# Optimization experiments

Measured on AMD Instinct MI355X. Metric: run time of the kernel, lower is better.

Reference implementation:

```python
import jax, jax.numpy as jnp
import numpy as np

NUM_HEADS = 16
DK = 64
DV = 64
MASK_FILL = -10000000000.0


def setup_inputs() -> dict:
    key = jax.random.key(0)
    kq, kk, kv, km = jax.random.split(key, 4)
    B, L, D = 2, 2048, NUM_HEADS * DK
    Q = jax.random.normal(kq, (B, L, D), dtype=jnp.float32)
    K = jax.random.normal(kk, (B, L, D), dtype=jnp.float32)
    V = jax.random.normal(kv, (B, L, NUM_HEADS * DV), dtype=jnp.float32)
    mask = jax.random.randint(km, (B, L, L), 0, 2).astype(jnp.bool_)
    return {"Q": Q, "K": K, "V": V, "mask": mask}


def reference(Q, K, V, mask):
    B, Lq, _ = Q.shape
    Lk = K.shape[1]
    # split heads: [B, H, L, d]
    q = Q.reshape(B, Lq, NUM_HEADS, DK).transpose(0, 2, 1, 3)
    k = K.reshape(B, Lk, NUM_HEADS, DK).transpose(0, 2, 1, 3)
    v = V.reshape(B, Lk, NUM_HEADS, DV).transpose(0, 2, 1, 3)
    # scores [B, H, Lq, Lk]; NOTE: original masks BEFORE scaling by 1/sqrt(dk)
    scores = jnp.einsum("bhqd,bhkd->bhqk", q, k)
    scores = jnp.where(mask[:, None, :, :], MASK_FILL, scores)
    scores = scores / jnp.sqrt(jnp.asarray(DK, dtype=scores.dtype))
    attn = jax.nn.softmax(scores, axis=-1)
    out = jnp.einsum("bhqk,bhkd->bhqd", attn, v)  # [B, H, Lq, dv]
    # concat heads back: [B, Lq, H*dv]
    return out.transpose(0, 2, 1, 3).reshape(B, Lq, NUM_HEADS * DV)
```

## Files before the change

### kernel.cpp

```cpp
#include <hip/hip_runtime.h>
#include <hip/hip_bf16.h>

#define NH 16
#define DH 64
#define LL 2048
#define DM 1024
#define SCALE2 0.1803368801111204f
#define GUARD_HI 60.0f
#define NT64 16

typedef __attribute__((ext_vector_type(4))) float f32x4;
typedef __attribute__((ext_vector_type(16))) float f32x16;
typedef __attribute__((ext_vector_type(8))) short bf16x8;

__device__ __forceinline__ unsigned pk2(float lo, float hi) {
    __hip_bfloat162 h = __float22bfloat162_rn(make_float2(lo, hi));
    union { __hip_bfloat162 h; unsigned u; } c; c.h = h; return c.u;
}
__device__ __forceinline__ bf16x8 cvt8(float4 a, float4 b) {
    union { bf16x8 v; unsigned u[4]; } r;
    r.u[0] = pk2(a.x, a.y); r.u[1] = pk2(a.z, a.w);
    r.u[2] = pk2(b.x, b.y); r.u[3] = pk2(b.z, b.w);
    return r.v;
}
__device__ __forceinline__ float exp2_fast(float x) {
    float y;
    asm("v_exp_f32 %0, %1" : "=v"(y) : "v"(x));
    return y;
}
__device__ __forceinline__ float keepf(float p, unsigned nw, int idx) {
    int k = (int)(nw << (31 - idx)) >> 31;
    unsigned pu = __builtin_bit_cast(unsigned, p) & (unsigned)k;
    return __builtin_bit_cast(float, pu);
}

__global__ __launch_bounds__(256) void pack_mask(const void* __restrict__ mask,
                                                 unsigned* __restrict__ bits)
{
    const int tid = threadIdx.x;
    const int lane = tid & 63;
    const int* mw = (const int*)mask;
    unsigned long long bad = __ballot((unsigned)mw[lane] > 1u);
    const bool is_int = (bad == 0ULL);

    const int wid = blockIdx.x * 256 + tid;
    const int kw = wid & 63;
    const int q64 = wid >> 6;
    unsigned m = 0;
    if (is_int) {
        const int* p = (const int*)mask + (size_t)q64 * LL + kw * 32;
        #pragma unroll
        for (int j = 0; j < 32; j += 4) {
            int4 v = *(const int4*)(p + j);
            m |= (v.x ? 1u : 0u) << j;
            m |= (v.y ? 1u : 0u) << (j + 1);
            m |= (v.z ? 1u : 0u) << (j + 2);
            m |= (v.w ? 1u : 0u) << (j + 3);
        }
    } else {
        const unsigned* p = (const unsigned*)((const unsigned char*)mask
                                              + (size_t)q64 * LL + kw * 32);
        #pragma unroll
        for (int j = 0; j < 8; ++j) {
            unsigned v = p[j];
            m |= (v & 1u) << (4 * j);
            m |= ((v >> 8) & 1u) << (4 * j + 1);
            m |= ((v >> 16) & 1u) << (4 * j + 2);
            m |= ((v >> 24) & 1u) << (4 * j + 3);
        }
    }
    bits[wid] = ~m;
}

__global__ __launch_bounds__(256) void prep_k(const float* __restrict__ K,
                                              short* __restrict__ Kb)
{
    const int kt = blockIdx.x, h = blockIdx.y, b = blockIdx.z;
    const int tid = threadIdx.x;
    const int key = tid >> 2;
    const int d16 = tid & 3;
    const float* src = K + ((size_t)b * LL + kt * 64 + key) * DM + h * DH + d16 * 16;
    float4 f0 = *(const float4*)(src);
    float4 f1 = *(const float4*)(src + 4);
    float4 f2 = *(const float4*)(src + 8);
    float4 f3 = *(const float4*)(src + 12);
    short* dst = Kb + (((size_t)(b * NH + h) * 32 + kt) << 12);
    const int base = d16 * 1024 + (key >> 5) * 512 + (key & 31) * 8;
    *(bf16x8*)&dst[base] = cvt8(f0, f1);
    *(bf16x8*)&dst[base + 256] = cvt8(f2, f3);
}

__global__ __launch_bounds__(256) void prep_v(const float* __restrict__ V,
                                              short* __restrict__ Vb)
{
    const int kt = blockIdx.x, h = blockIdx.y, b = blockIdx.z;
    const int tid = threadIdx.x;
    const int kp = tid & 31;
    const int dv8 = tid >> 5;
    const float* s0 = V + ((size_t)b * LL + kt * 64 + 2 * kp) * DM + h * DH + dv8 * 8;
    float4 a0 = *(const float4*)(s0);
    float4 a1 = *(const float4*)(s0 + 4);
    float4 b0 = *(const float4*)(s0 + DM);
    float4 b1 = *(const float4*)(s0 + DM + 4);
    float av[8] = {a0.x, a0.y, a0.z, a0.w, a1.x, a1.y, a1.z, a1.w};
    float bv[8] = {b0.x, b0.y, b0.z, b0.w, b1.x, b1.y, b1.z, b1.w};
    short* dst = Vb + (((size_t)(b * NH + h) * 32 + kt) << 12);
    const int key0 = 2 * kp;
    const int m = key0 >> 4;
    const int w16 = key0 & 15;
    const int hh = (w16 >> 2) & 1;
    const int i0 = (w16 & 3) + 4 * (w16 >> 3);
    #pragma unroll
    for (int j = 0; j < 8; ++j) {
        int dv = dv8 * 8 + j;
        int off = m * 1024 + (dv >> 5) * 512 + hh * 256 + (dv & 31) * 8 + i0;
        *(unsigned*)&dst[off] = pk2(av[j], bv[j]);
    }
}

__global__ __launch_bounds__(512, 4) void mha_fwd6(
    const float* __restrict__ Q, const short* __restrict__ Kb,
    const short* __restrict__ Vb, const unsigned* __restrict__ mbits,
    float* __restrict__ out)
{
    const int bid = blockIdx.x;
    const int xcd = bid & 7;
    const int j = bid >> 3;
    const int pair = xcd * 4 + (j >> 4);
    const int qblk = j & 15;
    const int hd = pair & 15;
    const int b = pair >> 4;

    const int tid = threadIdx.x;
    const int w = tid >> 6;
    const int g = w >> 2;
    const int wg = w & 3;
    const int lane = tid & 63;
    const int lq = lane & 31;
    const int hh = lane >> 5;

    const int qbase = qblk * 128 + wg * 32;

    __shared__ short smem[32768];
    #define KOFF(gg, cc) (((gg) * 2 + (cc)) * 4096)
    #define VOFF(gg, cc) (16384 + ((gg) * 2 + (cc)) * 4096)

    const short* Ktile0 = Kb + ((size_t)(b * NH + hd) << 17);
    const short* Vtile0 = Vb + ((size_t)(b * NH + hd) << 17);
    const unsigned* Mrow = mbits + ((size_t)b * LL + qbase + lq) * 64 + g * 32;

    uint2 mreg = *(const uint2*)(Mrow);
    {
        const short* kb_ = Ktile0 + (size_t)(g * 16) * 4096;
        const short* vb_ = Vtile0 + (size_t)(g * 16) * 4096;
        #pragma unroll
        for (int c = 0; c < 2; ++c) {
            __builtin_amdgcn_global_load_lds(
                (const unsigned*)(kb_ + wg * 1024 + c * 512 + lane * 8),
                (unsigned*)&smem[KOFF(g, 0) + wg * 1024 + c * 512], 16, 0, 0);
            __builtin_amdgcn_global_load_lds(
                (const unsigned*)(vb_ + wg * 1024 + c * 512 + lane * 8),
                (unsigned*)&smem[VOFF(g, 0) + wg * 1024 + c * 512], 16, 0, 0);
        }
    }

    bf16x8 qf[4];
    {
        const float* qp = Q + ((size_t)b * LL + qbase + lq) * DM + hd * DH + 8 * hh;
        #pragma unroll
        for (int d16 = 0; d16 < 4; ++d16) {
            float4 a = *(const float4*)(qp + 16 * d16);
            float4 c = *(const float4*)(qp + 16 * d16 + 4);
            a.x *= SCALE2; a.y *= SCALE2; a.z *= SCALE2; a.w *= SCALE2;
            c.x *= SCALE2; c.y *= SCALE2; c.z *= SCALE2; c.w *= SCALE2;
            qf[d16] = cvt8(a, c);
        }
    }

    f32x16 o0, o1;
    #pragma unroll
    for (int i = 0; i < 16; ++i) { o0[i] = 0.f; o1[i] = 0.f; }
    float l_own = 0.f;
    float m_shift = 0.f;
    const int sh4 = 4 * hh;

    asm volatile("s_waitcnt vmcnt(0)" ::: "memory");
    __builtin_amdgcn_s_barrier();

    #pragma unroll 2
    for (int t = 0; t < NT64; ++t) {
        const int cur = t & 1;
        const uint2 m2 = mreg;
        if (t + 1 < NT64) {
            mreg = *(const uint2*)(Mrow + 2 * (t + 1));
            const short* kb_ = Ktile0 + (size_t)(g * 16 + t + 1) * 4096;
            const short* vb_ = Vtile0 + (size_t)(g * 16 + t + 1) * 4096;
            #pragma unroll
            for (int c = 0; c < 2; ++c) {
                __builtin_amdgcn_global_load_lds(
                    (const unsigned*)(kb_ + wg * 1024 + c * 512 + lane * 8),
                    (unsigned*)&smem[KOFF(g, cur ^ 1) + wg * 1024 + c * 512], 16, 0, 0);
                __builtin_amdgcn_global_load_lds(
                    (const unsigned*)(vb_ + wg * 1024 + c * 512 + lane * 8),
                    (unsigned*)&smem[VOFF(g, cur ^ 1) + wg * 1024 + c * 512], 16, 0, 0);
            }
            asm volatile("s_waitcnt vmcnt(5)" ::: "memory");
        } else {
            asm volatile("s_waitcnt vmcnt(0)" ::: "memory");
        }
        __builtin_amdgcn_s_barrier();
        __builtin_amdgcn_sched_barrier(0);

        #pragma unroll
        for (int kb2 = 0; kb2 < 2; ++kb2) {
            f32x16 s;
            #pragma unroll
            for (int i = 0; i < 16; ++i) s[i] = 0.f;
            __builtin_amdgcn_s_setprio(1);
            #pragma unroll
            for (int d16 = 0; d16 < 4; ++d16) {
                bf16x8 kf = *(const bf16x8*)
                    &smem[KOFF(g, cur) + d16 * 1024 + kb2 * 512 + lane * 8];
                s = __builtin_amdgcn_mfma_f32_32x32x16_bf16(kf, qf[d16], s, 0, 0, 0);
            }
            __builtin_amdgcn_s_setprio(0);

            {
                float a0 = fmaxf(fmaxf(s[0], s[1]), fmaxf(s[2], s[3]));
                float a1 = fmaxf(fmaxf(s[4], s[5]), fmaxf(s[6], s[7]));
                float a2 = fmaxf(fmaxf(s[8], s[9]), fmaxf(s[10], s[11]));
                float a3 = fmaxf(fmaxf(s[12], s[13]), fmaxf(s[14], s[15]));
                float mx = fmaxf(fmaxf(a0, a1), fmaxf(a2, a3));
                if (__builtin_expect(m_shift != 0.0f, 0)) {
                    #pragma unroll
                    for (int r = 0; r < 16; ++r) s[r] -= m_shift;
                    mx -= m_shift;
                }
                if (!__all(mx <= GUARD_HI)) {
                    float tmax = fmaxf(mx, __shfl_xor(mx, 32, 64));
                    float shift = tmax - 30.0f;
                    m_shift += shift;
                    float alpha = exp2_fast(-shift);
                    #pragma unroll
                    for (int i = 0; i < 16; ++i) { o0[i] *= alpha; o1[i] *= alpha; }
                    l_own *= alpha;
                    #pragma unroll
                    for (int r = 0; r < 16; ++r) s[r] -= shift;
                }
            }

            const unsigned nw = (kb2 ? m2.y : m2.x) >> sh4;
            union { bf16x8 v; unsigned u[4]; } pa, pb;
            float lsum;
            {
                float p0 = keepf(exp2_fast(s[0]), nw, 0);
                float p1 = keepf(exp2_fast(s[1]), nw, 1);
                float p2 = keepf(exp2_fast(s[2]), nw, 2);
                float p3 = keepf(exp2_fast(s[3]), nw, 3);
                float p4 = keepf(exp2_fast(s[4]), nw, 8);
                float p5 = keepf(exp2_fast(s[5]), nw, 9);
                float p6 = keepf(exp2_fast(s[6]), nw, 10);
                float p7 = keepf(exp2_fast(s[7]), nw, 11);
                pa.u[0] = pk2(p0, p1); pa.u[1] = pk2(p2, p3);
                pa.u[2] = pk2(p4, p5); pa.u[3] = pk2(p6, p7);
                lsum = ((p0 + p1) + (p2 + p3)) + ((p4 + p5) + (p6 + p7));
            }
            {
                float p0 = keepf(exp2_fast(s[8]), nw, 16);
                float p1 = keepf(exp2_fast(s[9]), nw, 17);
                float p2 = keepf(exp2_fast(s[10]), nw, 18);
                float p3 = keepf(exp2_fast(s[11]), nw, 19);
                float p4 = keepf(exp2_fast(s[12]), nw, 24);
                float p5 = keepf(exp2_fast(s[13]), nw, 25);
                float p6 = keepf(exp2_fast(s[14]), nw, 26);
                float p7 = keepf(exp2_fast(s[15]), nw, 27);
                pb.u[0] = pk2(p0, p1); pb.u[1] = pk2(p2, p3);
                pb.u[2] = pk2(p4, p5); pb.u[3] = pk2(p6, p7);
                lsum += ((p0 + p1) + (p2 + p3)) + ((p4 + p5) + (p6 + p7));
            }
            l_own += lsum;

            __builtin_amdgcn_s_setprio(1);
            {
                const int m0 = kb2 * 2;
                bf16x8 v0 = *(const bf16x8*)&smem[VOFF(g, cur) + m0 * 1024 + lane * 8];
                bf16x8 v1 = *(const bf16x8*)&smem[VOFF(g, cur) + m0 * 1024 + 512 + lane * 8];
                o0 = __builtin_amdgcn_mfma_f32_32x32x16_bf16(v0, pa.v, o0, 0, 0, 0);
                o1 = __builtin_amdgcn_mfma_f32_32x32x16_bf16(v1, pa.v, o1, 0, 0, 0);
                bf16x8 v2 = *(const bf16x8*)&smem[VOFF(g, cur) + (m0 + 1) * 1024 + lane * 8];
                bf16x8 v3 = *(const bf16x8*)&smem[VOFF(g, cur) + (m0 + 1) * 1024 + 512 + lane * 8];
                o0 = __builtin_amdgcn_mfma_f32_32x32x16_bf16(v2, pb.v, o0, 0, 0, 0);
                o1 = __builtin_amdgcn_mfma_f32_32x32x16_bf16(v3, pb.v, o1, 0, 0, 0);
            }
            __builtin_amdgcn_s_setprio(0);
        }

        __builtin_amdgcn_sched_barrier(0);
        __builtin_amdgcn_s_barrier();
    }


    float* cb = (float*)smem;
    const int cbase = (wg * 64 + lane) * 34;
    if (g == 1) {
        #pragma unroll
        for (int i = 0; i < 16; ++i) { cb[cbase + i] = o0[i]; cb[cbase + 16 + i] = o1[i]; }
        cb[cbase + 32] = l_own;
        cb[cbase + 33] = m_shift;
    }
    __syncthreads();
    if (g == 0) {
        float msB = cb[cbase + 33];
        float lB = cb[cbase + 32];
        float M = fmaxf(m_shift, msB);
        float aA = exp2_fast(m_shift - M);
        float aB = exp2_fast(msB - M);
        float lc = l_own * aA + lB * aB;
        lc += __shfl_xor(lc, 32, 64);
        float inv = __builtin_amdgcn_rcpf(lc);
        #pragma unroll
        for (int i = 0; i < 16; ++i) {
            o0[i] = (o0[i] * aA + cb[cbase + i] * aB) * inv;
            o1[i] = (o1[i] * aA + cb[cbase + 16 + i] * aB) * inv;
        }
        float* fout = out + ((size_t)b * LL + qbase + lq) * DM + hd * DH + 4 * hh;
        #pragma unroll
        for (int rg = 0; rg < 4; ++rg) {
            float4 v0, v1;
            v0.x = o0[4 * rg + 0]; v0.y = o0[4 * rg + 1];
            v0.z = o0[4 * rg + 2]; v0.w = o0[4 * rg + 3];
            v1.x = o1[4 * rg + 0]; v1.y = o1[4 * rg + 1];
            v1.z = o1[4 * rg + 2]; v1.w = o1[4 * rg + 3];
            *(float4*)(fout + 8 * rg) = v0;
            *(float4*)(fout + 32 + 8 * rg) = v1;
        }
    }
    #undef KOFF
    #undef VOFF
}

extern "C" void kernel_launch(void* const* d_in, const int* in_sizes, int n_in,
                              void* d_out, int out_size, void* d_ws, size_t ws_size,
                              hipStream_t stream) {
    const float* Q = (const float*)d_in[0];
    const float* K = (const float*)d_in[1];
    const float* V = (const float*)d_in[2];
    const void* mask = d_in[3];
    float* out = (float*)d_out;

    unsigned* bits = (unsigned*)d_ws;
    const size_t MASK_B = (size_t)2 * LL * 64 * 4;
    const size_t KV_B = (size_t)2 * NH * 32 * 4096 * 2;
    short* Kb = (short*)((char*)d_ws + MASK_B);
    short* Vb = (short*)((char*)d_ws + MASK_B + KV_B);

    pack_mask<<<dim3(2 * LL * 64 / 256), dim3(256), 0, stream>>>(mask, bits);
    prep_k<<<dim3(32, NH, 2), dim3(256), 0, stream>>>(K, Kb);
    prep_v<<<dim3(32, NH, 2), dim3(256), 0, stream>>>(V, Vb);
    mha_fwd6<<<dim3(512), dim3(512), 0, stream>>>(Q, Kb, Vb, bits, out);
}
```

Before: 81.69 us.

## Split KV range across separate blocks and merge partials in a combine kernel

Replaces the in-block two-group KV split with a split-K scheme. Each 256-thread block handles one half of the key range and writes unnormalized partial outputs plus row sums and shifts to workspace. A new combine kernel rescales and merges the two halves. The aim is smaller blocks, twice as many of them, and no in-block LDS reduction, which should improve occupancy and scheduling. The cost is an extra 32 MB of partial writes and reads, one more kernel launch, and a single wait-then-barrier per tile in place of the earlier partial vmcnt overlap. The old kernel stays as a fallback when the workspace is too small.

```diff
diff --git a/kernel.cpp b/kernel.cpp
--- a/kernel.cpp
+++ b/kernel.cpp
@@ -7,7 +7,6 @@
 #define DM 1024
 #define SCALE2 0.1803368801111204f
 #define GUARD_HI 60.0f
-#define NT64 16
 
 typedef __attribute__((ext_vector_type(4))) float f32x4;
 typedef __attribute__((ext_vector_type(16))) float f32x16;
@@ -118,50 +117,43 @@
     }
 }
 
-__global__ __launch_bounds__(512, 4) void mha_fwd6(
+__global__ __launch_bounds__(256, 4) void mha_fwd7(
     const float* __restrict__ Q, const short* __restrict__ Kb,
     const short* __restrict__ Vb, const unsigned* __restrict__ mbits,
-    float* __restrict__ out)
+    float* __restrict__ part, float* __restrict__ lm)
 {
     const int bid = blockIdx.x;
     const int xcd = bid & 7;
     const int j = bid >> 3;
-    const int pair = xcd * 4 + (j >> 4);
-    const int qblk = j & 15;
+    const int pair = xcd * 4 + (j >> 5);
+    const int rem = j & 31;
+    const int qblk = rem >> 1;
+    const int half = rem & 1;
     const int hd = pair & 15;
     const int b = pair >> 4;
 
     const int tid = threadIdx.x;
-    const int w = tid >> 6;
-    const int g = w >> 2;
-    const int wg = w & 3;
+    const int wg = tid >> 6;
     const int lane = tid & 63;
     const int lq = lane & 31;
     const int hh = lane >> 5;
-
     const int qbase = qblk * 128 + wg * 32;
 
-    __shared__ short smem[32768];
-    #define KOFF(gg, cc) (((gg) * 2 + (cc)) * 4096)
-    #define VOFF(gg, cc) (16384 + ((gg) * 2 + (cc)) * 4096)
-
-    const short* Ktile0 = Kb + ((size_t)(b * NH + hd) << 17);
-    const short* Vtile0 = Vb + ((size_t)(b * NH + hd) << 17);
-    const unsigned* Mrow = mbits + ((size_t)b * LL + qbase + lq) * 64 + g * 32;
+    __shared__ short smem[16384];
+
+    const short* Ktile0 = Kb + ((size_t)(b * NH + hd) << 17) + ((size_t)(half * 16) << 12);
+    const short* Vtile0 = Vb + ((size_t)(b * NH + hd) << 17) + ((size_t)(half * 16) << 12);
+    const unsigned* Mrow = mbits + ((size_t)b * LL + qbase + lq) * 64 + half * 32;
 
     uint2 mreg = *(const uint2*)(Mrow);
-    {
-        const short* kb_ = Ktile0 + (size_t)(g * 16) * 4096;
-        const short* vb_ = Vtile0 + (size_t)(g * 16) * 4096;
-        #pragma unroll
-        for (int c = 0; c < 2; ++c) {
-            __builtin_amdgcn_global_load_lds(
-                (const unsigned*)(kb_ + wg * 1024 + c * 512 + lane * 8),
-                (unsigned*)&smem[KOFF(g, 0) + wg * 1024 + c * 512], 16, 0, 0);
-            __builtin_amdgcn_global_load_lds(
-                (const unsigned*)(vb_ + wg * 1024 + c * 512 + lane * 8),
-                (unsigned*)&smem[VOFF(g, 0) + wg * 1024 + c * 512], 16, 0, 0);
-        }
+    #pragma unroll
+    for (int c = 0; c < 2; ++c) {
+        __builtin_amdgcn_global_load_lds(
+            (const unsigned*)(Ktile0 + wg * 1024 + c * 512 + lane * 8),
+            (unsigned*)&smem[wg * 1024 + c * 512], 16, 0, 0);
+        __builtin_amdgcn_global_load_lds(
+            (const unsigned*)(Vtile0 + wg * 1024 + c * 512 + lane * 8),
+            (unsigned*)&smem[8192 + wg * 1024 + c * 512], 16, 0, 0);
     }
 
     bf16x8 qf[4];
@@ -184,31 +176,27 @@
     float m_shift = 0.f;
     const int sh4 = 4 * hh;
 
-    asm volatile("s_waitcnt vmcnt(0)" ::: "memory");
-    __builtin_amdgcn_s_barrier();
-
     #pragma unroll 2
-    for (int t = 0; t < NT64; ++t) {
+    for (int t = 0; t < 16; ++t) {
         const int cur = t & 1;
+        asm volatile("s_waitcnt vmcnt(0)" ::: "memory");
+        __builtin_amdgcn_s_barrier();
         const uint2 m2 = mreg;
-        if (t + 1 < NT64) {
+        if (t + 1 < 16) {
             mreg = *(const uint2*)(Mrow + 2 * (t + 1));
-            const short* kb_ = Ktile0 + (size_t)(g * 16 + t + 1) * 4096;
-            const short* vb_ = Vtile0 + (size_t)(g * 16 + t + 1) * 4096;
+            const short* kb_ = Ktile0 + (size_t)(t + 1) * 4096;
+            const short* vb_ = Vtile0 + (size_t)(t + 1) * 4096;
+            const int nb = (cur ^ 1) * 4096;
             #pragma unroll
             for (int c = 0; c < 2; ++c) {
                 __builtin_amdgcn_global_load_lds(
                     (const unsigned*)(kb_ + wg * 1024 + c * 512 + lane * 8),
-                    (unsigned*)&smem[KOFF(g, cur ^ 1) + wg * 1024 + c * 512], 16, 0, 0);
+                    (unsigned*)&smem[nb + wg * 1024 + c * 512], 16, 0, 0);
                 __builtin_amdgcn_global_load_lds(
                     (const unsigned*)(vb_ + wg * 1024 + c * 512 + lane * 8),
-                    (unsigned*)&smem[VOFF(g, cur ^ 1) + wg * 1024 + c * 512], 16, 0, 0);
-            }
-            asm volatile("s_waitcnt vmcnt(5)" ::: "memory");
-        } else {
-            asm volatile("s_waitcnt vmcnt(0)" ::: "memory");
-        }
-        __builtin_amdgcn_s_barrier();
+                    (unsigned*)&smem[8192 + nb + wg * 1024 + c * 512], 16, 0, 0);
+            }
+        }
         __builtin_amdgcn_sched_barrier(0);
 
         #pragma unroll
@@ -220,7 +208,7 @@
             #pragma unroll
             for (int d16 = 0; d16 < 4; ++d16) {
                 bf16x8 kf = *(const bf16x8*)
-                    &smem[KOFF(g, cur) + d16 * 1024 + kb2 * 512 + lane * 8];
+                    &smem[cur * 4096 + d16 * 1024 + kb2 * 512 + lane * 8];
                 s = __builtin_amdgcn_mfma_f32_32x32x16_bf16(kf, qf[d16], s, 0, 0, 0);
             }
             __builtin_amdgcn_s_setprio(0);
@@ -283,6 +271,232 @@
             __builtin_amdgcn_s_setprio(1);
             {
                 const int m0 = kb2 * 2;
+                const int vb0 = 8192 + cur * 4096;
+                bf16x8 v0 = *(const bf16x8*)&smem[vb0 + m0 * 1024 + lane * 8];
+                bf16x8 v1 = *(const bf16x8*)&smem[vb0 + m0 * 1024 + 512 + lane * 8];
+                o0 = __builtin_amdgcn_mfma_f32_32x32x16_bf16(v0, pa.v, o0, 0, 0, 0);
+                o1 = __builtin_amdgcn_mfma_f32_32x32x16_bf16(v1, pa.v, o1, 0, 0, 0);
+                bf16x8 v2 = *(const bf16x8*)&smem[vb0 + (m0 + 1) * 1024 + lane * 8];
+                bf16x8 v3 = *(const bf16x8*)&smem[vb0 + (m0 + 1) * 1024 + 512 + lane * 8];
+                o0 = __builtin_amdgcn_mfma_f32_32x32x16_bf16(v2, pb.v, o0, 0, 0, 0);
+                o1 = __builtin_amdgcn_mfma_f32_32x32x16_bf16(v3, pb.v, o1, 0, 0, 0);
+            }
+            __builtin_amdgcn_s_setprio(0);
+        }
+    }
+
+    l_own += __shfl_xor(l_own, 32, 64);
+    float* po = part + (size_t)half * (2 * (size_t)LL * DM)
+              + ((size_t)b * LL + qbase + lq) * DM + hd * DH + 4 * hh;
+    #pragma unroll
+    for (int rg = 0; rg < 4; ++rg) {
+        float4 v0, v1;
+        v0.x = o0[4 * rg + 0]; v0.y = o0[4 * rg + 1];
+        v0.z = o0[4 * rg + 2]; v0.w = o0[4 * rg + 3];
+        v1.x = o1[4 * rg + 0]; v1.y = o1[4 * rg + 1];
+        v1.z = o1[4 * rg + 2]; v1.w = o1[4 * rg + 3];
+        *(float4*)(po + 8 * rg) = v0;
+        *(float4*)(po + 32 + 8 * rg) = v1;
+    }
+    if (hh == 0) {
+        size_t li = ((((size_t)half * 2 + b) * NH + hd) * LL + (qbase + lq)) * 2;
+        lm[li] = l_own;
+        lm[li + 1] = m_shift;
+    }
+}
+
+__global__ __launch_bounds__(256) void combine(const float* __restrict__ part,
+                                               const float* __restrict__ lm,
+                                               float* __restrict__ out)
+{
+    const size_t idx = (size_t)blockIdx.x * 256 + threadIdx.x;
+    const size_t flat = idx * 4;
+    const int b = (int)(flat >> 21);
+    const int r = (int)(flat & 2097151);
+    const int q = r >> 10;
+    const int hd = (r & 1023) >> 6;
+    const size_t liA = (((size_t)b * NH + hd) * LL + q) * 2;
+    const size_t liB = (((size_t)(2 + b) * NH + hd) * LL + q) * 2;
+    float lA = lm[liA], mA = lm[liA + 1];
+    float lB = lm[liB], mB = lm[liB + 1];
+    float M = fmaxf(mA, mB);
+    float aA = exp2_fast(mA - M);
+    float aB = exp2_fast(mB - M);
+    float inv = __builtin_amdgcn_rcpf(lA * aA + lB * aB);
+    float4 oA = *(const float4*)(part + flat);
+    float4 oB = *(const float4*)(part + (size_t)4194304 + flat);
+    float4 o;
+    o.x = (oA.x * aA + oB.x * aB) * inv;
+    o.y = (oA.y * aA + oB.y * aB) * inv;
+    o.z = (oA.z * aA + oB.z * aB) * inv;
+    o.w = (oA.w * aA + oB.w * aB) * inv;
+    *(float4*)(out + flat) = o;
+}
+
+__global__ __launch_bounds__(512, 4) void mha_fwd6(
+    const float* __restrict__ Q, const short* __restrict__ Kb,
+    const short* __restrict__ Vb, const unsigned* __restrict__ mbits,
+    float* __restrict__ out)
+{
+    const int bid = blockIdx.x;
+    const int xcd = bid & 7;
+    const int j = bid >> 3;
+    const int pair = xcd * 4 + (j >> 4);
+    const int qblk = j & 15;
+    const int hd = pair & 15;
+    const int b = pair >> 4;
+
+    const int tid = threadIdx.x;
+    const int w = tid >> 6;
+    const int g = w >> 2;
+    const int wg = w & 3;
+    const int lane = tid & 63;
+    const int lq = lane & 31;
+    const int hh = lane >> 5;
+    const int qbase = qblk * 128 + wg * 32;
+
+    __shared__ short smem[32768];
+    #define KOFF(gg, cc) (((gg) * 2 + (cc)) * 4096)
+    #define VOFF(gg, cc) (16384 + ((gg) * 2 + (cc)) * 4096)
+
+    const short* Ktile0 = Kb + ((size_t)(b * NH + hd) << 17);
+    const short* Vtile0 = Vb + ((size_t)(b * NH + hd) << 17);
+    const unsigned* Mrow = mbits + ((size_t)b * LL + qbase + lq) * 64 + g * 32;
+
+    uint2 mreg = *(const uint2*)(Mrow);
+    {
+        const short* kb_ = Ktile0 + (size_t)(g * 16) * 4096;
+        const short* vb_ = Vtile0 + (size_t)(g * 16) * 4096;
+        #pragma unroll
+        for (int c = 0; c < 2; ++c) {
+            __builtin_amdgcn_global_load_lds(
+                (const unsigned*)(kb_ + wg * 1024 + c * 512 + lane * 8),
+                (unsigned*)&smem[KOFF(g, 0) + wg * 1024 + c * 512], 16, 0, 0);
+            __builtin_amdgcn_global_load_lds(
+                (const unsigned*)(vb_ + wg * 1024 + c * 512 + lane * 8),
+                (unsigned*)&smem[VOFF(g, 0) + wg * 1024 + c * 512], 16, 0, 0);
+        }
+    }
+
+    bf16x8 qf[4];
+    {
+        const float* qp = Q + ((size_t)b * LL + qbase + lq) * DM + hd * DH + 8 * hh;
+        #pragma unroll
+        for (int d16 = 0; d16 < 4; ++d16) {
+            float4 a = *(const float4*)(qp + 16 * d16);
+            float4 c = *(const float4*)(qp + 16 * d16 + 4);
+            a.x *= SCALE2; a.y *= SCALE2; a.z *= SCALE2; a.w *= SCALE2;
+            c.x *= SCALE2; c.y *= SCALE2; c.z *= SCALE2; c.w *= SCALE2;
+            qf[d16] = cvt8(a, c);
+        }
+    }
+
+    f32x16 o0, o1;
+    #pragma unroll
+    for (int i = 0; i < 16; ++i) { o0[i] = 0.f; o1[i] = 0.f; }
+    float l_own = 0.f;
+    float m_shift = 0.f;
+    const int sh4 = 4 * hh;
+
+    asm volatile("s_waitcnt vmcnt(0)" ::: "memory");
+    __builtin_amdgcn_s_barrier();
+
+    #pragma unroll 2
+    for (int t = 0; t < 16; ++t) {
+        const int cur = t & 1;
+        const uint2 m2 = mreg;
+        if (t + 1 < 16) {
+            mreg = *(const uint2*)(Mrow + 2 * (t + 1));
+            const short* kb_ = Ktile0 + (size_t)(g * 16 + t + 1) * 4096;
+            const short* vb_ = Vtile0 + (size_t)(g * 16 + t + 1) * 4096;
+            #pragma unroll
+            for (int c = 0; c < 2; ++c) {
+                __builtin_amdgcn_global_load_lds(
+                    (const unsigned*)(kb_ + wg * 1024 + c * 512 + lane * 8),
+                    (unsigned*)&smem[KOFF(g, cur ^ 1) + wg * 1024 + c * 512], 16, 0, 0);
+                __builtin_amdgcn_global_load_lds(
+                    (const unsigned*)(vb_ + wg * 1024 + c * 512 + lane * 8),
+                    (unsigned*)&smem[VOFF(g, cur ^ 1) + wg * 1024 + c * 512], 16, 0, 0);
+            }
+            asm volatile("s_waitcnt vmcnt(5)" ::: "memory");
+        } else {
+            asm volatile("s_waitcnt vmcnt(0)" ::: "memory");
+        }
+        __builtin_amdgcn_s_barrier();
+        __builtin_amdgcn_sched_barrier(0);
+
+        #pragma unroll
+        for (int kb2 = 0; kb2 < 2; ++kb2) {
+            f32x16 s;
+            #pragma unroll
+            for (int i = 0; i < 16; ++i) s[i] = 0.f;
+            __builtin_amdgcn_s_setprio(1);
+            #pragma unroll
+            for (int d16 = 0; d16 < 4; ++d16) {
+                bf16x8 kf = *(const bf16x8*)
+                    &smem[KOFF(g, cur) + d16 * 1024 + kb2 * 512 + lane * 8];
+                s = __builtin_amdgcn_mfma_f32_32x32x16_bf16(kf, qf[d16], s, 0, 0, 0);
+            }
+            __builtin_amdgcn_s_setprio(0);
+
+            {
+                float a0 = fmaxf(fmaxf(s[0], s[1]), fmaxf(s[2], s[3]));
+                float a1 = fmaxf(fmaxf(s[4], s[5]), fmaxf(s[6], s[7]));
+                float a2 = fmaxf(fmaxf(s[8], s[9]), fmaxf(s[10], s[11]));
+                float a3 = fmaxf(fmaxf(s[12], s[13]), fmaxf(s[14], s[15]));
+                float mx = fmaxf(fmaxf(a0, a1), fmaxf(a2, a3));
+                if (__builtin_expect(m_shift != 0.0f, 0)) {
+                    #pragma unroll
+                    for (int r = 0; r < 16; ++r) s[r] -= m_shift;
+                    mx -= m_shift;
+                }
+                if (!__all(mx <= GUARD_HI)) {
+                    float tmax = fmaxf(mx, __shfl_xor(mx, 32, 64));
+                    float shift = tmax - 30.0f;
+                    m_shift += shift;
+                    float alpha = exp2_fast(-shift);
+                    #pragma unroll
+                    for (int i = 0; i < 16; ++i) { o0[i] *= alpha; o1[i] *= alpha; }
+                    l_own *= alpha;
+                    #pragma unroll
+                    for (int r = 0; r < 16; ++r) s[r] -= shift;
+                }
+            }
+
+            const unsigned nw = (kb2 ? m2.y : m2.x) >> sh4;
+            union { bf16x8 v; unsigned u[4]; } pa, pb;
+            float lsum;
+            {
+                float p0 = keepf(exp2_fast(s[0]), nw, 0);
+                float p1 = keepf(exp2_fast(s[1]), nw, 1);
+                float p2 = keepf(exp2_fast(s[2]), nw, 2);
+                float p3 = keepf(exp2_fast(s[3]), nw, 3);
+                float p4 = keepf(exp2_fast(s[4]), nw, 8);
+                float p5 = keepf(exp2_fast(s[5]), nw, 9);
+                float p6 = keepf(exp2_fast(s[6]), nw, 10);
+                float p7 = keepf(exp2_fast(s[7]), nw, 11);
+                pa.u[0] = pk2(p0, p1); pa.u[1] = pk2(p2, p3);
+                pa.u[2] = pk2(p4, p5); pa.u[3] = pk2(p6, p7);
+                lsum = ((p0 + p1) + (p2 + p3)) + ((p4 + p5) + (p6 + p7));
+            }
+            {
+                float p0 = keepf(exp2_fast(s[8]), nw, 16);
+                float p1 = keepf(exp2_fast(s[9]), nw, 17);
+                float p2 = keepf(exp2_fast(s[10]), nw, 18);
+                float p3 = keepf(exp2_fast(s[11]), nw, 19);
+                float p4 = keepf(exp2_fast(s[12]), nw, 24);
+                float p5 = keepf(exp2_fast(s[13]), nw, 25);
+                float p6 = keepf(exp2_fast(s[14]), nw, 26);
+                float p7 = keepf(exp2_fast(s[15]), nw, 27);
+                pb.u[0] = pk2(p0, p1); pb.u[1] = pk2(p2, p3);
+                pb.u[2] = pk2(p4, p5); pb.u[3] = pk2(p6, p7);
+                lsum += ((p0 + p1) + (p2 + p3)) + ((p4 + p5) + (p6 + p7));
+            }
+            l_own += lsum;
+
+            __builtin_amdgcn_s_setprio(1);
+            {
+                const int m0 = kb2 * 2;
                 bf16x8 v0 = *(const bf16x8*)&smem[VOFF(g, cur) + m0 * 1024 + lane * 8];
                 bf16x8 v1 = *(const bf16x8*)&smem[VOFF(g, cur) + m0 * 1024 + 512 + lane * 8];
                 o0 = __builtin_amdgcn_mfma_f32_32x32x16_bf16(v0, pa.v, o0, 0, 0, 0);
@@ -298,7 +512,6 @@
         __builtin_amdgcn_sched_barrier(0);
         __builtin_amdgcn_s_barrier();
     }
-
 
     float* cb = (float*)smem;
     const int cbase = (wg * 64 + lane) * 34;
@@ -348,14 +561,26 @@
     const void* mask = d_in[3];
     float* out = (float*)d_out;
 
+    const size_t MASK_B = (size_t)2 * LL * 64 * 4;
+    const size_t K_B = (size_t)2 * NH * 32 * 4096 * 2;
+    const size_t V_B = K_B;
+    const size_t PART_B = (size_t)2 * 2 * LL * DM * 4;
+    const size_t LM_B = (size_t)4 * NH * LL * 2 * 4;
+
     unsigned* bits = (unsigned*)d_ws;
-    const size_t MASK_B = (size_t)2 * LL * 64 * 4;
-    const size_t KV_B = (size_t)2 * NH * 32 * 4096 * 2;
     short* Kb = (short*)((char*)d_ws + MASK_B);
-    short* Vb = (short*)((char*)d_ws + MASK_B + KV_B);
+    short* Vb = (short*)((char*)d_ws + MASK_B + K_B);
+    float* part = (float*)((char*)d_ws + MASK_B + K_B + V_B);
+    float* lm = (float*)((char*)d_ws + MASK_B + K_B + V_B + PART_B);
 
     pack_mask<<<dim3(2 * LL * 64 / 256), dim3(256), 0, stream>>>(mask, bits);
     prep_k<<<dim3(32, NH, 2), dim3(256), 0, stream>>>(K, Kb);
     prep_v<<<dim3(32, NH, 2), dim3(256), 0, stream>>>(V, Vb);
-    mha_fwd6<<<dim3(512), dim3(512), 0, stream>>>(Q, Kb, Vb, bits, out);
-}
+
+    if (ws_size >= MASK_B + K_B + V_B + PART_B + LM_B) {
+        mha_fwd7<<<dim3(1024), dim3(256), 0, stream>>>(Q, Kb, Vb, bits, part, lm);
+        combine<<<dim3(4096), dim3(256), 0, stream>>>(part, lm, out);
+    } else {
+        mha_fwd6<<<dim3(512), dim3(512), 0, stream>>>(Q, Kb, Vb, bits, out);
+    }
+}
```

After: 91.94 us. 12.5% more time.

## Split keys four ways across blocks with fp16 partials and a combine kernel

Applied to the files above, without the earlier changes.

The attention kernel now splits the key range into four quarters, each handled by its own 256-thread block over 32-key tiles. This replaces the old two-group in-block split and its LDS merge, giving 2048 smaller blocks instead of 512. Partial outputs for quarters 1-3 go to fp16 workspace along with per-row sums and shifts, and a new combine4 kernel rescales and merges them into the final output. The K and V prep kernels are fused into one launch with a 32-key tile layout. This adds parallelism and occupancy, at the cost of extra global traffic for the partials, an extra launch, and fp16 precision loss in the partial results.

```diff
diff --git a/kernel.cpp b/kernel.cpp
--- a/kernel.cpp
+++ b/kernel.cpp
@@ -7,7 +7,6 @@
 #define DM 1024
 #define SCALE2 0.1803368801111204f
 #define GUARD_HI 60.0f
-#define NT64 16
 
 typedef __attribute__((ext_vector_type(4))) float f32x4;
 typedef __attribute__((ext_vector_type(16))) float f32x16;
@@ -72,97 +71,88 @@
     bits[wid] = ~m;
 }
 
-__global__ __launch_bounds__(256) void prep_k(const float* __restrict__ K,
-                                              short* __restrict__ Kb)
+__global__ __launch_bounds__(256) void prep_kv(const float* __restrict__ K,
+                                               const float* __restrict__ V,
+                                               short* __restrict__ Kb,
+                                               short* __restrict__ Vb)
 {
-    const int kt = blockIdx.x, h = blockIdx.y, b = blockIdx.z;
+    const int kt = blockIdx.x;
+    const int h = blockIdx.y, b = blockIdx.z;
     const int tid = threadIdx.x;
-    const int key = tid >> 2;
-    const int d16 = tid & 3;
-    const float* src = K + ((size_t)b * LL + kt * 64 + key) * DM + h * DH + d16 * 16;
-    float4 f0 = *(const float4*)(src);
-    float4 f1 = *(const float4*)(src + 4);
-    float4 f2 = *(const float4*)(src + 8);
-    float4 f3 = *(const float4*)(src + 12);
-    short* dst = Kb + (((size_t)(b * NH + h) * 32 + kt) << 12);
-    const int base = d16 * 1024 + (key >> 5) * 512 + (key & 31) * 8;
-    *(bf16x8*)&dst[base] = cvt8(f0, f1);
-    *(bf16x8*)&dst[base + 256] = cvt8(f2, f3);
-}
-
-__global__ __launch_bounds__(256) void prep_v(const float* __restrict__ V,
-                                              short* __restrict__ Vb)
-{
-    const int kt = blockIdx.x, h = blockIdx.y, b = blockIdx.z;
-    const int tid = threadIdx.x;
-    const int kp = tid & 31;
-    const int dv8 = tid >> 5;
-    const float* s0 = V + ((size_t)b * LL + kt * 64 + 2 * kp) * DM + h * DH + dv8 * 8;
-    float4 a0 = *(const float4*)(s0);
-    float4 a1 = *(const float4*)(s0 + 4);
-    float4 b0 = *(const float4*)(s0 + DM);
-    float4 b1 = *(const float4*)(s0 + DM + 4);
-    float av[8] = {a0.x, a0.y, a0.z, a0.w, a1.x, a1.y, a1.z, a1.w};
-    float bv[8] = {b0.x, b0.y, b0.z, b0.w, b1.x, b1.y, b1.z, b1.w};
-    short* dst = Vb + (((size_t)(b * NH + h) * 32 + kt) << 12);
-    const int key0 = 2 * kp;
-    const int m = key0 >> 4;
-    const int w16 = key0 & 15;
-    const int hh = (w16 >> 2) & 1;
-    const int i0 = (w16 & 3) + 4 * (w16 >> 3);
-    #pragma unroll
-    for (int j = 0; j < 8; ++j) {
-        int dv = dv8 * 8 + j;
-        int off = m * 1024 + (dv >> 5) * 512 + hh * 256 + (dv & 31) * 8 + i0;
-        *(unsigned*)&dst[off] = pk2(av[j], bv[j]);
-    }
-}
-
-__global__ __launch_bounds__(512, 4) void mha_fwd6(
+    if (tid < 128) {
+        const int key = tid >> 2;
+        const int d16 = tid & 3;
+        const float* src = K + ((size_t)b * LL + kt * 32 + key) * DM + h * DH + d16 * 16;
+        float4 f0 = *(const float4*)(src);
+        float4 f1 = *(const float4*)(src + 4);
+        float4 f2 = *(const float4*)(src + 8);
+        float4 f3 = *(const float4*)(src + 12);
+        short* dst = Kb + (((size_t)(b * NH + h) * 64 + kt) << 11);
+        const int base = d16 * 512 + key * 8;
+        *(bf16x8*)&dst[base] = cvt8(f0, f1);
+        *(bf16x8*)&dst[base + 256] = cvt8(f2, f3);
+    } else {
+        const int vt = tid - 128;
+        const int kp = vt & 15;
+        const int dv8 = vt >> 4;
+        const float* s0 = V + ((size_t)b * LL + kt * 32 + 2 * kp) * DM + h * DH + dv8 * 8;
+        float4 a0 = *(const float4*)(s0);
+        float4 a1 = *(const float4*)(s0 + 4);
+        float4 b0 = *(const float4*)(s0 + DM);
+        float4 b1 = *(const float4*)(s0 + DM + 4);
+        float av[8] = {a0.x, a0.y, a0.z, a0.w, a1.x, a1.y, a1.z, a1.w};
+        float bv[8] = {b0.x, b0.y, b0.z, b0.w, b1.x, b1.y, b1.z, b1.w};
+        short* dst = Vb + (((size_t)(b * NH + h) * 64 + kt) << 11);
+        const int key0 = 2 * kp;
+        const int m = key0 >> 4;
+        const int w16 = key0 & 15;
+        const int hh = (w16 >> 2) & 1;
+        const int i0 = (w16 & 3) + 4 * (w16 >> 3);
+        #pragma unroll
+        for (int j = 0; j < 8; ++j) {
+            int dv = dv8 * 8 + j;
+            int off = m * 1024 + (dv >> 5) * 512 + hh * 256 + (dv & 31) * 8 + i0;
+            *(unsigned*)&dst[off] = pk2(av[j], bv[j]);
+        }
+    }
+}
+
+__global__ __launch_bounds__(256, 8) void mha_fwd8(
     const float* __restrict__ Q, const short* __restrict__ Kb,
     const short* __restrict__ Vb, const unsigned* __restrict__ mbits,
-    float* __restrict__ out)
+    float* __restrict__ out, _Float16* __restrict__ part,
+    float* __restrict__ lm)
 {
     const int bid = blockIdx.x;
     const int xcd = bid & 7;
     const int j = bid >> 3;
-    const int pair = xcd * 4 + (j >> 4);
-    const int qblk = j & 15;
+    const int pair = xcd * 4 + (j >> 6);
+    const int rem = j & 63;
+    const int qblk = rem >> 2;
+    const int quarter = rem & 3;
     const int hd = pair & 15;
     const int b = pair >> 4;
 
     const int tid = threadIdx.x;
-    const int w = tid >> 6;
-    const int g = w >> 2;
-    const int wg = w & 3;
+    const int wg = tid >> 6;
     const int lane = tid & 63;
     const int lq = lane & 31;
     const int hh = lane >> 5;
-
     const int qbase = qblk * 128 + wg * 32;
 
-    __shared__ short smem[32768];
-    #define KOFF(gg, cc) (((gg) * 2 + (cc)) * 4096)
-    #define VOFF(gg, cc) (16384 + ((gg) * 2 + (cc)) * 4096)
-
-    const short* Ktile0 = Kb + ((size_t)(b * NH + hd) << 17);
-    const short* Vtile0 = Vb + ((size_t)(b * NH + hd) << 17);
-    const unsigned* Mrow = mbits + ((size_t)b * LL + qbase + lq) * 64 + g * 32;
-
-    uint2 mreg = *(const uint2*)(Mrow);
-    {
-        const short* kb_ = Ktile0 + (size_t)(g * 16) * 4096;
-        const short* vb_ = Vtile0 + (size_t)(g * 16) * 4096;
-        #pragma unroll
-        for (int c = 0; c < 2; ++c) {
-            __builtin_amdgcn_global_load_lds(
-                (const unsigned*)(kb_ + wg * 1024 + c * 512 + lane * 8),
-                (unsigned*)&smem[KOFF(g, 0) + wg * 1024 + c * 512], 16, 0, 0);
-            __builtin_amdgcn_global_load_lds(
-                (const unsigned*)(vb_ + wg * 1024 + c * 512 + lane * 8),
-                (unsigned*)&smem[VOFF(g, 0) + wg * 1024 + c * 512], 16, 0, 0);
-        }
-    }
+    __shared__ short smem[8192];
+
+    const short* Ktile0 = Kb + ((size_t)(b * NH + hd) << 17) + ((size_t)(quarter * 16) << 11);
+    const short* Vtile0 = Vb + ((size_t)(b * NH + hd) << 17) + ((size_t)(quarter * 16) << 11);
+    const unsigned* Mrow = mbits + ((size_t)b * LL + qbase + lq) * 64 + quarter * 16;
+
+    unsigned mreg = Mrow[0];
+    __builtin_amdgcn_global_load_lds(
+        (const unsigned*)(Ktile0 + wg * 512 + lane * 8),
+        (unsigned*)&smem[wg * 512], 16, 0, 0);
+    __builtin_amdgcn_global_load_lds(
+        (const unsigned*)(Vtile0 + wg * 512 + lane * 8),
+        (unsigned*)&smem[4096 + wg * 512], 16, 0, 0);
 
     bf16x8 qf[4];
     {
@@ -184,145 +174,116 @@
     float m_shift = 0.f;
     const int sh4 = 4 * hh;
 
-    asm volatile("s_waitcnt vmcnt(0)" ::: "memory");
-    __builtin_amdgcn_s_barrier();
-
     #pragma unroll 2
-    for (int t = 0; t < NT64; ++t) {
+    for (int t = 0; t < 16; ++t) {
         const int cur = t & 1;
-        const uint2 m2 = mreg;
-        if (t + 1 < NT64) {
-            mreg = *(const uint2*)(Mrow + 2 * (t + 1));
-            const short* kb_ = Ktile0 + (size_t)(g * 16 + t + 1) * 4096;
-            const short* vb_ = Vtile0 + (size_t)(g * 16 + t + 1) * 4096;
-            #pragma unroll
-            for (int c = 0; c < 2; ++c) {
-                __builtin_amdgcn_global_load_lds(
-                    (const unsigned*)(kb_ + wg * 1024 + c * 512 + lane * 8),
-                    (unsigned*)&smem[KOFF(g, cur ^ 1) + wg * 1024 + c * 512], 16, 0, 0);
-                __builtin_amdgcn_global_load_lds(
-                    (const unsigned*)(vb_ + wg * 1024 + c * 512 + lane * 8),
-                    (unsigned*)&smem[VOFF(g, cur ^ 1) + wg * 1024 + c * 512], 16, 0, 0);
+        asm volatile("s_waitcnt vmcnt(0)" ::: "memory");
+        __builtin_amdgcn_s_barrier();
+        const unsigned mword = mreg;
+        if (t + 1 < 16) {
+            mreg = Mrow[t + 1];
+            const short* kb_ = Ktile0 + (size_t)(t + 1) * 2048;
+            const short* vb_ = Vtile0 + (size_t)(t + 1) * 2048;
+            const int nb = (cur ^ 1) * 2048;
+            __builtin_amdgcn_global_load_lds(
+                (const unsigned*)(kb_ + wg * 512 + lane * 8),
+                (unsigned*)&smem[nb + wg * 512], 16, 0, 0);
+            __builtin_amdgcn_global_load_lds(
+                (const unsigned*)(vb_ + wg * 512 + lane * 8),
+                (unsigned*)&smem[4096 + nb + wg * 512], 16, 0, 0);
+        }
+        __builtin_amdgcn_sched_barrier(0);
+
+        f32x16 s;
+        #pragma unroll
+        for (int i = 0; i < 16; ++i) s[i] = 0.f;
+        __builtin_amdgcn_s_setprio(1);
+        #pragma unroll
+        for (int d16 = 0; d16 < 4; ++d16) {
+            bf16x8 kf = *(const bf16x8*)&smem[cur * 2048 + d16 * 512 + lane * 8];
+            s = __builtin_amdgcn_mfma_f32_32x32x16_bf16(kf, qf[d16], s, 0, 0, 0);
+        }
+        __builtin_amdgcn_s_setprio(0);
+
+        {
+            float a0 = fmaxf(fmaxf(s[0], s[1]), fmaxf(s[2], s[3]));
+            float a1 = fmaxf(fmaxf(s[4], s[5]), fmaxf(s[6], s[7]));
+            float a2 = fmaxf(fmaxf(s[8], s[9]), fmaxf(s[10], s[11]));
+            float a3 = fmaxf(fmaxf(s[12], s[13]), fmaxf(s[14], s[15]));
+            float mx = fmaxf(fmaxf(a0, a1), fmaxf(a2, a3));
+            if (__builtin_expect(m_shift != 0.0f, 0)) {
+                #pragma unroll
+                for (int r = 0; r < 16; ++r) s[r] -= m_shift;
+                mx -= m_shift;
             }
-            asm volatile("s_waitcnt vmcnt(5)" ::: "memory");
-        } else {
-            asm volatile("s_waitcnt vmcnt(0)" ::: "memory");
-        }
-        __builtin_amdgcn_s_barrier();
-        __builtin_amdgcn_sched_barrier(0);
-
-        #pragma unroll
-        for (int kb2 = 0; kb2 < 2; ++kb2) {
-            f32x16 s;
-            #pragma unroll
-            for (int i = 0; i < 16; ++i) s[i] = 0.f;
-            __builtin_amdgcn_s_setprio(1);
-            #pragma unroll
-            for (int d16 = 0; d16 < 4; ++d16) {
-                bf16x8 kf = *(const bf16x8*)
-                    &smem[KOFF(g, cur) + d16 * 1024 + kb2 * 512 + lane * 8];
-                s = __builtin_amdgcn_mfma_f32_32x32x16_bf16(kf, qf[d16], s, 0, 0, 0);
+            if (!__all(mx <= GUARD_HI)) {
+                float tmax = fmaxf(mx, __shfl_xor(mx, 32, 64));
+                float shift = tmax - 30.0f;
+                m_shift += shift;
+                float alpha = exp2_fast(-shift);
+                #pragma unroll
+                for (int i = 0; i < 16; ++i) { o0[i] *= alpha; o1[i] *= alpha; }
+                l_own *= alpha;
+                #pragma unroll
+                for (int r = 0; r < 16; ++r) s[r] -= shift;
             }
-            __builtin_amdgcn_s_setprio(0);
-
-            {
-                float a0 = fmaxf(fmaxf(s[0], s[1]), fmaxf(s[2], s[3]));
-                float a1 = fmaxf(fmaxf(s[4], s[5]), fmaxf(s[6], s[7]));
-                float a2 = fmaxf(fmaxf(s[8], s[9]), fmaxf(s[10], s[11]));
-                float a3 = fmaxf(fmaxf(s[12], s[13]), fmaxf(s[14], s[15]));
-                float mx = fmaxf(fmaxf(a0, a1), fmaxf(a2, a3));
-                if (__builtin_expect(m_shift != 0.0f, 0)) {
-                    #pragma unroll
-                    for (int r = 0; r < 16; ++r) s[r] -= m_shift;
-                    mx -= m_shift;
-                }
-                if (!__all(mx <= GUARD_HI)) {
-                    float tmax = fmaxf(mx, __shfl_xor(mx, 32, 64));
-                    float shift = tmax - 30.0f;
-                    m_shift += shift;
-                    float alpha = exp2_fast(-shift);
-                    #pragma unroll
-                    for (int i = 0; i < 16; ++i) { o0[i] *= alpha; o1[i] *= alpha; }
-                    l_own *= alpha;
-                    #pragma unroll
-                    for (int r = 0; r < 16; ++r) s[r] -= shift;
-                }
-            }
-
-            const unsigned nw = (kb2 ? m2.y : m2.x) >> sh4;
-            union { bf16x8 v; unsigned u[4]; } pa, pb;
-            float lsum;
-            {
-                float p0 = keepf(exp2_fast(s[0]), nw, 0);
-                float p1 = keepf(exp2_fast(s[1]), nw, 1);
-                float p2 = keepf(exp2_fast(s[2]), nw, 2);
-                float p3 = keepf(exp2_fast(s[3]), nw, 3);
-                float p4 = keepf(exp2_fast(s[4]), nw, 8);
-                float p5 = keepf(exp2_fast(s[5]), nw, 9);
-                float p6 = keepf(exp2_fast(s[6]), nw, 10);
-                float p7 = keepf(exp2_fast(s[7]), nw, 11);
-                pa.u[0] = pk2(p0, p1); pa.u[1] = pk2(p2, p3);
-                pa.u[2] = pk2(p4, p5); pa.u[3] = pk2(p6, p7);
-                lsum = ((p0 + p1) + (p2 + p3)) + ((p4 + p5) + (p6 + p7));
-            }
-            {
-                float p0 = keepf(exp2_fast(s[8]), nw, 16);
-                float p1 = keepf(exp2_fast(s[9]), nw, 17);
-                float p2 = keepf(exp2_fast(s[10]), nw, 18);
-                float p3 = keepf(exp2_fast(s[11]), nw, 19);
-                float p4 = keepf(exp2_fast(s[12]), nw, 24);
-                float p5 = keepf(exp2_fast(s[13]), nw, 25);
-                float p6 = keepf(exp2_fast(s[14]), nw, 26);
-                float p7 = keepf(exp2_fast(s[15]), nw, 27);
-                pb.u[0] = pk2(p0, p1); pb.u[1] = pk2(p2, p3);
-                pb.u[2] = pk2(p4, p5); pb.u[3] = pk2(p6, p7);
-                lsum += ((p0 + p1) + (p2 + p3)) + ((p4 + p5) + (p6 + p7));
-            }
-            l_own += lsum;
-
-            __builtin_amdgcn_s_setprio(1);
-            {
-                const int m0 = kb2 * 2;
-                bf16x8 v0 = *(const bf16x8*)&smem[VOFF(g, cur) + m0 * 1024 + lane * 8];
-                bf16x8 v1 = *(const bf16x8*)&smem[VOFF(g, cur) + m0 * 1024 + 512 + lane * 8];
-                o0 = __builtin_amdgcn_mfma_f32_32x32x16_bf16(v0, pa.v, o0, 0, 0, 0);
-                o1 = __builtin_amdgcn_mfma_f32_32x32x16_bf16(v1, pa.v, o1, 0, 0, 0);
-                bf16x8 v2 = *(const bf16x8*)&smem[VOFF(g, cur) + (m0 + 1) * 1024 + lane * 8];
-                bf16x8 v3 = *(const bf16x8*)&smem[VOFF(g, cur) + (m0 + 1) * 1024 + 512 + lane * 8];
-                o0 = __builtin_amdgcn_mfma_f32_32x32x16_bf16(v2, pb.v, o0, 0, 0, 0);
-                o1 = __builtin_amdgcn_mfma_f32_32x32x16_bf16(v3, pb.v, o1, 0, 0, 0);
-            }
-            __builtin_amdgcn_s_setprio(0);
-        }
-
-        __builtin_amdgcn_sched_barrier(0);
-        __builtin_amdgcn_s_barrier();
-    }
-
-
-    float* cb = (float*)smem;
-    const int cbase = (wg * 64 + lane) * 34;
-    if (g == 1) {
-        #pragma unroll
-        for (int i = 0; i < 16; ++i) { cb[cbase + i] = o0[i]; cb[cbase + 16 + i] = o1[i]; }
-        cb[cbase + 32] = l_own;
-        cb[cbase + 33] = m_shift;
-    }
-    __syncthreads();
-    if (g == 0) {
-        float msB = cb[cbase + 33];
-        float lB = cb[cbase + 32];
-        float M = fmaxf(m_shift, msB);
-        float aA = exp2_fast(m_shift - M);
-        float aB = exp2_fast(msB - M);
-        float lc = l_own * aA + lB * aB;
-        lc += __shfl_xor(lc, 32, 64);
-        float inv = __builtin_amdgcn_rcpf(lc);
-        #pragma unroll
-        for (int i = 0; i < 16; ++i) {
-            o0[i] = (o0[i] * aA + cb[cbase + i] * aB) * inv;
-            o1[i] = (o1[i] * aA + cb[cbase + 16 + i] * aB) * inv;
-        }
+        }
+
+        const unsigned nw = mword >> sh4;
+        union { bf16x8 v; unsigned u[4]; } pa, pb;
+        float lsum;
+        {
+            float p0 = keepf(exp2_fast(s[0]), nw, 0);
+            float p1 = keepf(exp2_fast(s[1]), nw, 1);
+            float p2 = keepf(exp2_fast(s[2]), nw, 2);
+            float p3 = keepf(exp2_fast(s[3]), nw, 3);
+            float p4 = keepf(exp2_fast(s[4]), nw, 8);
+            float p5 = keepf(exp2_fast(s[5]), nw, 9);
+            float p6 = keepf(exp2_fast(s[6]), nw, 10);
+            float p7 = keepf(exp2_fast(s[7]), nw, 11);
+            pa.u[0] = pk2(p0, p1); pa.u[1] = pk2(p2, p3);
+            pa.u[2] = pk2(p4, p5); pa.u[3] = pk2(p6, p7);
+            lsum = ((p0 + p1) + (p2 + p3)) + ((p4 + p5) + (p6 + p7));
+        }
+        {
+            float p0 = keepf(exp2_fast(s[8]), nw, 16);
+            float p1 = keepf(exp2_fast(s[9]), nw, 17);
+            float p2 = keepf(exp2_fast(s[10]), nw, 18);
+            float p3 = keepf(exp2_fast(s[11]), nw, 19);
+            float p4 = keepf(exp2_fast(s[12]), nw, 24);
+            float p5 = keepf(exp2_fast(s[13]), nw, 25);
+            float p6 = keepf(exp2_fast(s[14]), nw, 26);
+            float p7 = keepf(exp2_fast(s[15]), nw, 27);
+            pb.u[0] = pk2(p0, p1); pb.u[1] = pk2(p2, p3);
+            pb.u[2] = pk2(p4, p5); pb.u[3] = pk2(p6, p7);
+            lsum += ((p0 + p1) + (p2 + p3)) + ((p4 + p5) + (p6 + p7));
+        }
+        l_own += lsum;
+
+        __builtin_amdgcn_s_setprio(1);
+        {
+            const int vb0 = 4096 + cur * 2048;
+            bf16x8 v0 = *(const bf16x8*)&smem[vb0 + 0 * 1024 + 0 * 512 + lane * 8];
+            bf16x8 v1 = *(const bf16x8*)&smem[vb0 + 0 * 1024 + 1 * 512 + lane * 8];
+            o0 = __builtin_amdgcn_mfma_f32_32x32x16_bf16(v0, pa.v, o0, 0, 0, 0);
+            o1 = __builtin_amdgcn_mfma_f32_32x32x16_bf16(v1, pa.v, o1, 0, 0, 0);
+            bf16x8 v2 = *(const bf16x8*)&smem[vb0 + 1 * 1024 + 0 * 512 + lane * 8];
+            bf16x8 v3 = *(const bf16x8*)&smem[vb0 + 1 * 1024 + 1 * 512 + lane * 8];
+            o0 = __builtin_amdgcn_mfma_f32_32x32x16_bf16(v2, pb.v, o0, 0, 0, 0);
+            o1 = __builtin_amdgcn_mfma_f32_32x32x16_bf16(v3, pb.v, o1, 0, 0, 0);
+        }
+        __builtin_amdgcn_s_setprio(0);
+    }
+
+    l_own += __shfl_xor(l_own, 32, 64);
+    if (__builtin_expect(l_own > 32768.f, 0)) {
+        const float sc = 2.3283064365386963e-10f;
+        l_own *= sc;
+        m_shift += 32.f;
+        #pragma unroll
+        for (int i = 0; i < 16; ++i) { o0[i] *= sc; o1[i] *= sc; }
+    }
+    if (quarter == 0) {
         float* fout = out + ((size_t)b * LL + qbase + lq) * DM + hd * DH + 4 * hh;
         #pragma unroll
         for (int rg = 0; rg < 4; ++rg) {
@@ -334,9 +295,70 @@
             *(float4*)(fout + 8 * rg) = v0;
             *(float4*)(fout + 32 + 8 * rg) = v1;
         }
-    }
-    #undef KOFF
-    #undef VOFF
+    } else {
+        _Float16* po = part + ((size_t)(quarter - 1) * 2 + b) * ((size_t)LL * DM)
+                     + (size_t)(qbase + lq) * DM + hd * DH + 4 * hh;
+        union H4 { _Float16 h[4]; short4 s; };
+        #pragma unroll
+        for (int rg = 0; rg < 4; ++rg) {
+            H4 u0, u1;
+            #pragma unroll
+            for (int jj = 0; jj < 4; ++jj) {
+                u0.h[jj] = (_Float16)o0[4 * rg + jj];
+                u1.h[jj] = (_Float16)o1[4 * rg + jj];
+            }
+            *(short4*)(po + 8 * rg) = u0.s;
+            *(short4*)(po + 32 + 8 * rg) = u1.s;
+        }
+    }
+    if (hh == 0) {
+        size_t li = ((((size_t)quarter * 2 + b) * NH + hd) * LL + (qbase + lq)) * 2;
+        lm[li] = l_own;
+        lm[li + 1] = m_shift;
+    }
+}
+
+__global__ __launch_bounds__(256) void combine4(const _Float16* __restrict__ part,
+                                                const float* __restrict__ lm,
+                                                float* __restrict__ out)
+{
+    const size_t idx = (size_t)blockIdx.x * 256 + threadIdx.x;
+    const size_t flat = idx * 4;
+    const int b = (int)(flat >> 21);
+    const int r = (int)(flat & 2097151);
+    const int q = r >> 10;
+    const int col = r & 1023;
+    const int hd = col >> 6;
+
+    float l[4], m[4];
+    #pragma unroll
+    for (int s = 0; s < 4; ++s) {
+        size_t li = ((((size_t)s * 2 + b) * NH + hd) * LL + q) * 2;
+        l[s] = lm[li];
+        m[s] = lm[li + 1];
+    }
+    float M = fmaxf(fmaxf(m[0], m[1]), fmaxf(m[2], m[3]));
+    float a[4];
+    #pragma unroll
+    for (int s = 0; s < 4; ++s) a[s] = exp2_fast(m[s] - M);
+    float denom = l[0] * a[0] + l[1] * a[1] + l[2] * a[2] + l[3] * a[3];
+    float inv = __builtin_amdgcn_rcpf(denom);
+
+    float4 acc = *(const float4*)(out + flat);
+    acc.x *= a[0]; acc.y *= a[0]; acc.z *= a[0]; acc.w *= a[0];
+    #pragma unroll
+    for (int s = 1; s < 4; ++s) {
+        const _Float16* ph = part + ((size_t)(s - 1) * 2 + b) * ((size_t)LL * DM)
+                           + (size_t)q * DM + col;
+        union H4 { short4 s4; _Float16 h[4]; } u;
+        u.s4 = *(const short4*)(ph);
+        acc.x += (float)u.h[0] * a[s];
+        acc.y += (float)u.h[1] * a[s];
+        acc.z += (float)u.h[2] * a[s];
+        acc.w += (float)u.h[3] * a[s];
+    }
+    acc.x *= inv; acc.y *= inv; acc.z *= inv; acc.w *= inv;
+    *(float4*)(out + flat) = acc;
 }
 
 extern "C" void kernel_launch(void* const* d_in, const int* in_sizes, int n_in,
@@ -348,14 +370,20 @@
     const void* mask = d_in[3];
     float* out = (float*)d_out;
 
+    const size_t MASK_B = (size_t)2 * LL * 64 * 4;
+    const size_t K_B = (size_t)2 * NH * 64 * 2048 * 2;
+    const size_t V_B = K_B;
+    const size_t PART_B = (size_t)3 * 2 * LL * DM * 2;
+    const size_t LM_B = (size_t)4 * 2 * NH * LL * 2 * 4;
+
     unsigned* bits = (unsigned*)d_ws;
-    const size_t MASK_B = (size_t)2 * LL * 64 * 4;
-    const size_t KV_B = (size_t)2 * NH * 32 * 4096 * 2;
     short* Kb = (short*)((char*)d_ws + MASK_B);
-    short* Vb = (short*)((char*)d_ws + MASK_B + KV_B);
+    short* Vb = (short*)((char*)d_ws + MASK_B + K_B);
+    _Float16* part = (_Float16*)((char*)d_ws + MASK_B + K_B + V_B);
+    float* lm = (float*)((char*)d_ws + MASK_B + K_B + V_B + PART_B);
 
     pack_mask<<<dim3(2 * LL * 64 / 256), dim3(256), 0, stream>>>(mask, bits);
-    prep_k<<<dim3(32, NH, 2), dim3(256), 0, stream>>>(K, Kb);
-    prep_v<<<dim3(32, NH, 2), dim3(256), 0, stream>>>(V, Vb);
-    mha_fwd6<<<dim3(512), dim3(512), 0, stream>>>(Q, Kb, Vb, bits, out);
-}
+    prep_kv<<<dim3(64, NH, 2), dim3(256), 0, stream>>>(K, V, Kb, Vb);
+    mha_fwd8<<<dim3(2048), dim3(256), 0, stream>>>(Q, Kb, Vb, bits, out, part, lm);
+    combine4<<<dim3(4096), dim3(256), 0, stream>>>(part, lm, out);
+}
```

New measurement: 267.6 us. 228% more time.
